# Kernel optimization log

Measured on AMD Instinct MI355X. Metric: run time of the kernel, lower is better.

## Reference

```python
import jax, jax.numpy as jnp
import numpy as np

N = 50000
E = 800000
D_IN = 128
D_HID = 256


def setup_inputs() -> dict:
    key = jax.random.key(0)
    ks = jax.random.split(key, 9)
    x = jax.random.normal(ks[0], (N, D_IN), dtype=jnp.float32)
    edge_index = jax.random.randint(ks[1], (2, E), 0, N, dtype=jnp.int64)
    edge_weight = jax.random.uniform(ks[2], (E,), dtype=jnp.float32)
    # GCNConv params (lin: y = x @ W.T, plus bias added after aggregation)
    W1 = jax.random.normal(ks[3], (D_HID, D_IN), dtype=jnp.float32) / np.sqrt(D_IN)
    b1 = jnp.zeros((D_HID,), dtype=jnp.float32)
    W2 = jax.random.normal(ks[4], (D_IN, D_HID), dtype=jnp.float32) / np.sqrt(D_HID)
    b2 = jnp.zeros((D_IN,), dtype=jnp.float32)
    gamma = jnp.ones((D_IN,), dtype=jnp.float32)
    beta = jnp.zeros((D_IN,), dtype=jnp.float32)
    return {"x": x, "edge_index": edge_index, "edge_weight": edge_weight,
            "W1": W1, "b1": b1, "W2": W2, "b2": b2,
            "gamma": gamma, "beta": beta}


def _gcn_norm(edge_index, edge_weight, n_nodes):
    # add self loops with weight 1.0 (PyG gcn_norm default)
    loop = jnp.arange(n_nodes, dtype=edge_index.dtype)
    src = jnp.concatenate([edge_index[0], loop])
    dst = jnp.concatenate([edge_index[1], loop])
    w = jnp.concatenate([edge_weight, jnp.ones((n_nodes,), edge_weight.dtype)])
    # symmetric normalization: deg over target index
    deg = jax.ops.segment_sum(w, dst, num_segments=n_nodes)
    dinv = jnp.where(deg > 0, jax.lax.rsqrt(deg), 0.0)
    norm = dinv[src] * w * dinv[dst]
    return src, dst, norm


def _gcn_conv(x, src, dst, norm, W, b, n_nodes):
    h = x @ W.T                                    # [N, out]
    msg = h[src] * norm[:, None]                   # gather + scale [E+N, out]
    out = jax.ops.segment_sum(msg, dst, num_segments=n_nodes)
    return out + b


def reference(x, edge_index, edge_weight, W1, b1, W2, b2, gamma, beta):
    n_nodes = x.shape[0]
    src, dst, norm = _gcn_norm(edge_index, edge_weight, n_nodes)
    h = _gcn_conv(x, src, dst, norm, W1, b1, n_nodes)
    h = jax.nn.relu(h)
    h = _gcn_conv(h, src, dst, norm, W2, b2, n_nodes)
    # LayerNorm over last dim
    mu = jnp.mean(h, axis=-1, keepdims=True)
    var = jnp.mean(jnp.square(h - mu), axis=-1, keepdims=True)
    h = (h - mu) * jax.lax.rsqrt(var + 1e-5) * gamma + beta
    return h
```

## Files before the change

kernel.cpp:

```cpp
#include <hip/hip_runtime.h>

typedef unsigned short ushort_t;
typedef __attribute__((ext_vector_type(8))) short short8;
typedef __attribute__((ext_vector_type(8))) unsigned short u16x8;
typedef __attribute__((ext_vector_type(4))) float float4v;

#define MAXDEG 48

__device__ inline float b2f(ushort_t u) {
    unsigned x = ((unsigned)u) << 16;
    return __builtin_bit_cast(float, x);
}
__device__ inline ushort_t f2b(float f) {
    unsigned x = __builtin_bit_cast(unsigned, f);
    unsigned r = (x + 0x7fffu + ((x >> 16) & 1u)) >> 16;
    return (ushort_t)r;
}

__device__ inline void load_edge(const int* __restrict__ ei, int e, int E,
                                 int& s, int& d) {
    int ec = min(e, E - 1);
    int2 c64 = ((const int2*)ei)[ec];
    unsigned long long m = __ballot(c64.y != 0);
    if (m != 0ull) {
        s = ei[ec];
        d = ei[(size_t)E + ec];
    } else {
        s = c64.x;
        d = ((const int2*)ei)[(size_t)E + ec].x;
    }
}


__global__ __launch_bounds__(256) void k_mega(const int* __restrict__ ei,
                                              const float* __restrict__ w,
                                              const float* __restrict__ x,
                                              const float* __restrict__ W1,
                                              const float* __restrict__ W2,
                                              unsigned* packed,
                                              unsigned* __restrict__ edata,
                                              ushort_t* __restrict__ xb_raw,
                                              ushort_t* __restrict__ W1b,
                                              ushort_t* __restrict__ W2b,
                                              int E, int Nn, int gE, int gX) {
    int b = blockIdx.x;
    bool isEdge;
    int widx;
    if (3 * gE <= (int)gridDim.x) {
        if (b < 3 * gE) {
            if (b % 3 == 0) { isEdge = true;  widx = b / 3; }
            else            { isEdge = false; widx = b - b / 3 - 1; }
        } else {
            isEdge = false; widx = b - gE;
        }
    } else {
        isEdge = b < gE;
        widx = isEdge ? b : b - gE;
    }

    if (isEdge) {
        int e = widx * 256 + threadIdx.x;
        int s, d;
        load_edge(ei, e, E, s, d);
        if (e < E) {
            if ((unsigned)s < (unsigned)Nn && (unsigned)d < (unsigned)Nn) {
                float wv = w[e];
                unsigned fx = (unsigned)(wv * 65536.0f + 0.5f);
                unsigned old = atomicAdd(packed + d, (1u << 22) | fx);
                int r = (int)(old >> 22);
                if (r < MAXDEG) {
                    unsigned wq = (unsigned)(wv * 32768.0f + 0.5f);
                    wq = min(wq, 32767u);
                    edata[(size_t)d * MAXDEG + r] = ((unsigned)s << 15) | wq;
                }
            }
        }
    } else if (widx < gX) {
        int i = widx * 256 + threadIdx.x;
        if (i < Nn * 32) {
            float4v v = ((const float4v*)x)[i];
            ushort4 o;
            o.x = f2b(v[0]); o.y = f2b(v[1]); o.z = f2b(v[2]); o.w = f2b(v[3]);
            ((ushort4*)xb_raw)[i] = o;
        }
    } else {
        int i = (widx - gX) * 256 + threadIdx.x;
        if (i < 32768) W1b[i] = f2b(W1[i]);
        else if (i < 65536) W2b[i - 32768] = f2b(W2[i - 32768]);
    }
}


__global__ __launch_bounds__(256) void k_xscale(const ushort_t* __restrict__ xb_raw,
                                                const unsigned* __restrict__ packed,
                                                float* __restrict__ dinv,
                                                ushort_t* __restrict__ xb, int Nn) {
    int v = (blockIdx.x * blockDim.x + threadIdx.x) >> 5;
    int hl = threadIdx.x & 31;
    if (v >= Nn) return;
    unsigned pk = packed[v];
    float dv = rsqrtf(1.0f + (float)(pk & 0x3FFFFFu) * (1.0f / 65536.0f));
    if (hl == 0) dinv[v] = dv;
    ushort4 xr = ((const ushort4*)(xb_raw + (size_t)v * 128))[hl];
    ushort4 o;
    o.x = f2b(b2f(xr.x) * dv); o.y = f2b(b2f(xr.y) * dv);
    o.z = f2b(b2f(xr.z) * dv); o.w = f2b(b2f(xr.w) * dv);
    ((ushort4*)(xb + (size_t)v * 128))[hl] = o;
}


__device__ inline void agg_edges(const ushort_t* __restrict__ src,
                                 const unsigned* __restrict__ ed, int n,
                                 int ld, int pg, float* a) {
    for (int i = 0; i < n; i += 16) {
        unsigned e2[8];
#pragma unroll
        for (int j = 0; j < 8; ++j) e2[j] = ed[min(i + 2 * j + pg, n - 1)];
        u16x8 q[8];
        float nw[8];
#pragma unroll
        for (int j = 0; j < 8; ++j) {
            int sN = (int)(e2[j] >> 15);
            q[j] = ((const u16x8*)(src + (size_t)sN * 128))[ld];
            nw[j] = (i + 2 * j + pg < n)
                        ? (float)(e2[j] & 0x7FFFu) * (1.0f / 32768.0f)
                        : 0.f;
        }
#pragma unroll
        for (int j = 0; j < 8; ++j)
#pragma unroll
            for (int k = 0; k < 8; ++k)
                a[k] += b2f((ushort_t)q[j][k]) * nw[j];
    }
}


__global__ __launch_bounds__(256) void k_agg1(const ushort_t* __restrict__ xb,
                                              const unsigned* __restrict__ packed,
                                              const unsigned* __restrict__ edata,
                                              ushort_t* __restrict__ ax, int Nn) {
    int v = (blockIdx.x * blockDim.x + threadIdx.x) >> 5;
    int hl = threadIdx.x & 31;
    if (v >= Nn) return;
    int pg = hl >> 4, ld = hl & 15;
    unsigned pk = packed[v];
    float dv = rsqrtf(1.0f + (float)(pk & 0x3FFFFFu) * (1.0f / 65536.0f));
    float a[8] = {0.f, 0.f, 0.f, 0.f, 0.f, 0.f, 0.f, 0.f};
    if (pg == 0) {
        u16x8 pq = ((const u16x8*)(xb + (size_t)v * 128))[ld];
#pragma unroll
        for (int k = 0; k < 8; ++k) a[k] = b2f((ushort_t)pq[k]);
    }
    int n = min((int)(pk >> 22), MAXDEG);
    agg_edges(xb, edata + (size_t)v * MAXDEG, n, ld, pg, a);
#pragma unroll
    for (int k = 0; k < 8; ++k) {
        a[k] += __shfl_xor(a[k], 16);
        a[k] *= dv;
    }
    if (pg == 0) {
        u16x8 o;
#pragma unroll
        for (int k = 0; k < 8; ++k) o[k] = f2b(a[k]);
        ((u16x8*)(ax + (size_t)v * 128))[ld] = o;
    }
}


__global__ __launch_bounds__(256, 2) void k_gemm_fused(const ushort_t* __restrict__ ax,
                                                       const ushort_t* __restrict__ W1b,
                                                       const float* __restrict__ b1v,
                                                       const ushort_t* __restrict__ W2b,
                                                       const float* __restrict__ dinv,
                                                       ushort_t* __restrict__ h2, int Nn) {
    __shared__ ushort_t tile[64][264];
    int tid = threadIdx.x, wid = tid >> 6, lane = tid & 63;
    int m = lane & 15, q = lane >> 4;
    int blk = blockIdx.x * 64;

    short8 wf[4][4];
#pragma unroll
    for (int nt = 0; nt < 4; ++nt) {
        const ushort_t* wb = W1b + (size_t)(wid * 64 + nt * 16 + m) * 128 + q * 8;
#pragma unroll
        for (int kt = 0; kt < 4; ++kt) wf[nt][kt] = *(const short8*)(wb + kt * 32);
    }
    short8 af[4][4];
#pragma unroll
    for (int mi = 0; mi < 4; ++mi) {
        int arow = blk + mi * 16 + m;
        bool rv = arow < Nn;
        const ushort_t* ab = ax + (size_t)arow * 128 + q * 8;
#pragma unroll
        for (int kt = 0; kt < 4; ++kt)
            af[mi][kt] = rv ? *(const short8*)(ab + kt * 32) : (short8)0;
    }

    float4v acc1[4][4];
#pragma unroll
    for (int mi = 0; mi < 4; ++mi)
#pragma unroll
        for (int nt = 0; nt < 4; ++nt) acc1[mi][nt] = (float4v){0.f, 0.f, 0.f, 0.f};

#pragma unroll
    for (int kt = 0; kt < 4; ++kt)
#pragma unroll
        for (int mi = 0; mi < 4; ++mi)
#pragma unroll
            for (int nt = 0; nt < 4; ++nt)
                acc1[mi][nt] = __builtin_amdgcn_mfma_f32_16x16x32_bf16(
                    af[mi][kt], wf[nt][kt], acc1[mi][nt], 0, 0, 0);

#pragma unroll
    for (int nt = 0; nt < 4; ++nt) {
        int col = wid * 64 + nt * 16 + m;
        float bb = b1v[col];
#pragma unroll
        for (int mi = 0; mi < 4; ++mi) {
#pragma unroll
            for (int r = 0; r < 4; ++r) {
                float v = acc1[mi][nt][r] + bb;
                v = v > 0.f ? v : 0.f;
                tile[mi * 16 + q * 4 + r][col] = f2b(v);
            }
        }
    }
    __syncthreads();

    short8 w2f[2][8];
#pragma unroll
    for (int n2 = 0; n2 < 2; ++n2) {
        const ushort_t* wb = W2b + (size_t)(wid * 32 + n2 * 16 + m) * 256 + q * 8;
#pragma unroll
        for (int kt = 0; kt < 8; ++kt) w2f[n2][kt] = *(const short8*)(wb + kt * 32);
    }

    float4v acc2[4][2];
#pragma unroll
    for (int mi = 0; mi < 4; ++mi)
#pragma unroll
        for (int n2 = 0; n2 < 2; ++n2) acc2[mi][n2] = (float4v){0.f, 0.f, 0.f, 0.f};

#pragma unroll
    for (int kt = 0; kt < 8; ++kt) {
#pragma unroll
        for (int mi = 0; mi < 4; ++mi) {
            short8 a2 = *(const short8*)&tile[mi * 16 + m][kt * 32 + q * 8];
#pragma unroll
            for (int n2 = 0; n2 < 2; ++n2)
                acc2[mi][n2] = __builtin_amdgcn_mfma_f32_16x16x32_bf16(
                    a2, w2f[n2][kt], acc2[mi][n2], 0, 0, 0);
        }
    }

    float drow[4][4];
#pragma unroll
    for (int mi = 0; mi < 4; ++mi)
#pragma unroll
        for (int r = 0; r < 4; ++r) {
            int row = blk + mi * 16 + q * 4 + r;
            drow[mi][r] = (row < Nn) ? dinv[row] : 0.f;
        }

#pragma unroll
    for (int mi = 0; mi < 4; ++mi) {
#pragma unroll
        for (int n2 = 0; n2 < 2; ++n2) {
            int col = wid * 32 + n2 * 16 + m;
#pragma unroll
            for (int r = 0; r < 4; ++r) {
                int row = blk + mi * 16 + q * 4 + r;
                if (row < Nn)
                    h2[(size_t)row * 128 + col] = f2b(acc2[mi][n2][r] * drow[mi][r]);
            }
        }
    }
}


__global__ __launch_bounds__(256) void k_agg2_ln(const ushort_t* __restrict__ h2,
                                                 const unsigned* __restrict__ packed,
                                                 const unsigned* __restrict__ edata,
                                                 const float* __restrict__ b2v,
                                                 const float* __restrict__ gv,
                                                 const float* __restrict__ bev,
                                                 float* __restrict__ out, int Nn) {
    int v = (blockIdx.x * blockDim.x + threadIdx.x) >> 5;
    int hl = threadIdx.x & 31;
    if (v >= Nn) return;
    int pg = hl >> 4, ld = hl & 15;
    unsigned pk = packed[v];
    float dv = rsqrtf(1.0f + (float)(pk & 0x3FFFFFu) * (1.0f / 65536.0f));
    float a[8] = {0.f, 0.f, 0.f, 0.f, 0.f, 0.f, 0.f, 0.f};
    if (pg == 0) {
        u16x8 pq = ((const u16x8*)(h2 + (size_t)v * 128))[ld];
#pragma unroll
        for (int k = 0; k < 8; ++k) a[k] = b2f((ushort_t)pq[k]);
    }
    int n = min((int)(pk >> 22), MAXDEG);
    agg_edges(h2, edata + (size_t)v * MAXDEG, n, ld, pg, a);

    int d0 = ld * 8;
#pragma unroll
    for (int k = 0; k < 8; ++k) {
        a[k] += __shfl_xor(a[k], 16);
        a[k] = a[k] * dv + b2v[d0 + k];
    }

    float ssum = 0.f, ssq = 0.f;
#pragma unroll
    for (int k = 0; k < 8; ++k) { ssum += a[k]; ssq += a[k] * a[k]; }
#pragma unroll
    for (int off = 1; off < 32; off <<= 1) {
        ssum += __shfl_xor(ssum, off);
        ssq += __shfl_xor(ssq, off);
    }
    float mu = ssum * (1.0f / 256.0f);
    float var = ssq * (1.0f / 256.0f) - mu * mu;
    float r = rsqrtf(var + 1e-5f);
    if (pg == 0) {
        float4v o1, o2;
#pragma unroll
        for (int k = 0; k < 4; ++k) {
            o1[k] = (a[k] - mu) * r * gv[d0 + k] + bev[d0 + k];
            o2[k] = (a[k + 4] - mu) * r * gv[d0 + 4 + k] + bev[d0 + 4 + k];
        }
        float4v* op = (float4v*)(out + (size_t)v * 128 + d0);
        op[0] = o1;
        op[1] = o2;
    }
}


extern "C" void kernel_launch(void* const* d_in, const int* in_sizes, int n_in,
                              void* d_out, int out_size, void* d_ws, size_t ws_size,
                              hipStream_t stream) {
    const float* x   = (const float*)d_in[0];
    const int*   ei  = (const int*)d_in[1];
    const float* ew  = (const float*)d_in[2];
    const float* W1  = (const float*)d_in[3];
    const float* b1v = (const float*)d_in[4];
    const float* W2  = (const float*)d_in[5];
    const float* b2v = (const float*)d_in[6];
    const float* gv  = (const float*)d_in[7];
    const float* bev = (const float*)d_in[8];
    float* out = (float*)d_out;

    const int Nn = in_sizes[0] / 128;
    const int E  = in_sizes[2];

    char* base = (char*)d_ws;
    size_t off = 0;
    auto alloc = [&](size_t bytes) {
        char* p = base + off;
        off = (off + bytes + 255) & ~(size_t)255;
        return p;
    };
    unsigned* packed = (unsigned*)alloc((size_t)Nn * 4);
    float*    dinv   = (float*)alloc((size_t)Nn * 4);
    unsigned* edata  = (unsigned*)alloc((size_t)Nn * MAXDEG * 4);
    ushort_t* xb     = (ushort_t*)alloc((size_t)Nn * 128 * 2);
    ushort_t* h2     = (ushort_t*)alloc((size_t)Nn * 128 * 2);
    ushort_t* W1b    = (ushort_t*)alloc(32768 * 2);
    ushort_t* W2b    = (ushort_t*)alloc(32768 * 2);
    ushort_t* ax     = (ushort_t*)d_out;
    ushort_t* xb_raw = (ushort_t*)d_out + (size_t)Nn * 128;
    (void)ws_size; (void)n_in; (void)out_size;

    int gE = (E + 255) / 256;
    int gX = (Nn * 32 + 255) / 256;
    int gW = (Nn + 7) / 8;
    int gG = (Nn + 63) / 64;

    hipMemsetAsync(packed, 0, (size_t)Nn * 4, stream);
    k_mega<<<gE + gX + 256, 256, 0, stream>>>(ei, ew, x, W1, W2, packed, edata,
                                              xb_raw, W1b, W2b, E, Nn, gE, gX);
    k_xscale<<<gW, 256, 0, stream>>>(xb_raw, packed, dinv, xb, Nn);
    k_agg1<<<gW, 256, 0, stream>>>(xb, packed, edata, ax, Nn);
    k_gemm_fused<<<gG, 256, 0, stream>>>(ax, W1b, b1v, W2b, dinv, h2, Nn);
    k_agg2_ln<<<gW, 256, 0, stream>>>(h2, packed, edata, b2v, gv, bev, out, Nn);
}
```

Baseline: 225.6 us.

## Split layer-1 aggregation into four feature-column passes for L2 locality

After: 240.6 us. +6.7%, slower.

```diff
diff --git a/kernel.cpp b/kernel.cpp
--- a/kernel.cpp
+++ b/kernel.cpp
@@ -109,6 +109,65 @@
 }
 
 
+__global__ __launch_bounds__(256) void k_agg1(const ushort_t* __restrict__ xb,
+                                              const unsigned* __restrict__ packed,
+                                              const unsigned* __restrict__ edata,
+                                              ushort_t* __restrict__ ax,
+                                              int Nn, int gW) {
+    int bb = blockIdx.x;
+    int p  = bb / gW;
+    int nb = bb - p * gW;
+    int v  = (nb * 256 + threadIdx.x) >> 5;
+    int hl = threadIdx.x & 31;
+    if (v >= Nn) return;
+    int eg = hl >> 2;
+    int c  = hl & 3;
+    unsigned pk = packed[v];
+    float dv = rsqrtf(1.0f + (float)(pk & 0x3FFFFFu) * (1.0f / 65536.0f));
+    int n = min((int)(pk >> 22), MAXDEG);
+    const unsigned* ed = edata + (size_t)v * MAXDEG;
+    const ushort_t* base = xb + (size_t)p * 32 + (size_t)c * 8;
+
+    float a[8] = {0.f, 0.f, 0.f, 0.f, 0.f, 0.f, 0.f, 0.f};
+    if (eg == 0) {
+        u16x8 pq = *(const u16x8*)(base + (size_t)v * 128);
+#pragma unroll
+        for (int k = 0; k < 8; ++k) a[k] = b2f((ushort_t)pq[k]);
+    }
+    for (int i = 0; i < n; i += 32) {
+        unsigned e2[4];
+        u16x8 q[4];
+        float nw[4];
+#pragma unroll
+        for (int u = 0; u < 4; ++u) {
+            int idx = i + u * 8 + eg;
+            e2[u] = ed[min(idx, n - 1)];
+            int sN = (int)(e2[u] >> 15);
+            q[u] = *(const u16x8*)(base + (size_t)sN * 128);
+            nw[u] = (idx < n) ? (float)(e2[u] & 0x7FFFu) * (1.0f / 32768.0f) : 0.f;
+        }
+#pragma unroll
+        for (int u = 0; u < 4; ++u)
+#pragma unroll
+            for (int k = 0; k < 8; ++k)
+                a[k] += b2f((ushort_t)q[u][k]) * nw[u];
+    }
+#pragma unroll
+    for (int k = 0; k < 8; ++k) {
+        a[k] += __shfl_xor(a[k], 4);
+        a[k] += __shfl_xor(a[k], 8);
+        a[k] += __shfl_xor(a[k], 16);
+        a[k] *= dv;
+    }
+    if (eg == 0) {
+        u16x8 o;
+#pragma unroll
+        for (int k = 0; k < 8; ++k) o[k] = f2b(a[k]);
+        *(u16x8*)(ax + (size_t)v * 128 + (size_t)p * 32 + (size_t)c * 8) = o;
+    }
+}
+
+
 __device__ inline void agg_edges(const ushort_t* __restrict__ src,
                                  const unsigned* __restrict__ ed, int n,
                                  int ld, int pg, float* a) {
@@ -131,38 +190,6 @@
 #pragma unroll
             for (int k = 0; k < 8; ++k)
                 a[k] += b2f((ushort_t)q[j][k]) * nw[j];
-    }
-}
-
-
-__global__ __launch_bounds__(256) void k_agg1(const ushort_t* __restrict__ xb,
-                                              const unsigned* __restrict__ packed,
-                                              const unsigned* __restrict__ edata,
-                                              ushort_t* __restrict__ ax, int Nn) {
-    int v = (blockIdx.x * blockDim.x + threadIdx.x) >> 5;
-    int hl = threadIdx.x & 31;
-    if (v >= Nn) return;
-    int pg = hl >> 4, ld = hl & 15;
-    unsigned pk = packed[v];
-    float dv = rsqrtf(1.0f + (float)(pk & 0x3FFFFFu) * (1.0f / 65536.0f));
-    float a[8] = {0.f, 0.f, 0.f, 0.f, 0.f, 0.f, 0.f, 0.f};
-    if (pg == 0) {
-        u16x8 pq = ((const u16x8*)(xb + (size_t)v * 128))[ld];
-#pragma unroll
-        for (int k = 0; k < 8; ++k) a[k] = b2f((ushort_t)pq[k]);
-    }
-    int n = min((int)(pk >> 22), MAXDEG);
-    agg_edges(xb, edata + (size_t)v * MAXDEG, n, ld, pg, a);
-#pragma unroll
-    for (int k = 0; k < 8; ++k) {
-        a[k] += __shfl_xor(a[k], 16);
-        a[k] *= dv;
-    }
-    if (pg == 0) {
-        u16x8 o;
-#pragma unroll
-        for (int k = 0; k < 8; ++k) o[k] = f2b(a[k]);
-        ((u16x8*)(ax + (size_t)v * 128))[ld] = o;
     }
 }
 
@@ -376,7 +403,7 @@
     k_mega<<<gE + gX + 256, 256, 0, stream>>>(ei, ew, x, W1, W2, packed, edata,
                                               xb_raw, W1b, W2b, E, Nn, gE, gX);
     k_xscale<<<gW, 256, 0, stream>>>(xb_raw, packed, dinv, xb, Nn);
-    k_agg1<<<gW, 256, 0, stream>>>(xb, packed, edata, ax, Nn);
+    k_agg1<<<4 * gW, 256, 0, stream>>>(xb, packed, edata, ax, Nn, gW);
     k_gemm_fused<<<gG, 256, 0, stream>>>(ax, W1b, b1v, W2b, dinv, h2, Nn);
     k_agg2_ln<<<gW, 256, 0, stream>>>(h2, packed, edata, b2v, gv, bev, out, Nn);
 }
```
